# Kernel optimization log

Measured on AMD Instinct MI355X. Metric: run time of the kernel, lower is better.

## Reference

```python
import jax, jax.numpy as jnp
import numpy as np

N_NODES = 100000
N_EDGES = 3200000
IN_DIM = 20
HIDDEN = 4096
OUT_DIM = 2
BN_EPS = 1e-5


def setup_inputs() -> dict:
    key = jax.random.key(0)
    ks = jax.random.split(key, 6)
    node_feature = jax.random.normal(ks[0], (N_NODES, IN_DIM), dtype=jnp.float32)
    edge_index = jax.random.randint(ks[1], (2, N_EDGES), 0, N_NODES, dtype=jnp.int64)
    gcn_w = jax.random.normal(ks[2], (IN_DIM, HIDDEN), dtype=jnp.float32) * (1.0 / np.sqrt(IN_DIM))
    gcn_b = jax.random.normal(ks[3], (HIDDEN,), dtype=jnp.float32) * 0.01
    bn_gamma = jnp.ones((HIDDEN,), dtype=jnp.float32)
    bn_beta = jnp.zeros((HIDDEN,), dtype=jnp.float32)
    lin_w = jax.random.normal(ks[4], (HIDDEN, OUT_DIM), dtype=jnp.float32) * (1.0 / np.sqrt(HIDDEN))
    lin_b = jnp.zeros((OUT_DIM,), dtype=jnp.float32)
    return {"node_feature": node_feature, "edge_index": edge_index,
            "gcn_w": gcn_w, "gcn_b": gcn_b, "bn_gamma": bn_gamma,
            "bn_beta": bn_beta, "lin_w": lin_w, "lin_b": lin_b}


def reference(node_feature, edge_index, gcn_w, gcn_b, bn_gamma, bn_beta, lin_w, lin_b):
    n = node_feature.shape[0]
    # --- GCNConv: add self loops, symmetric degree normalization ---
    loop = jnp.arange(n, dtype=edge_index.dtype)
    row = jnp.concatenate([edge_index[0], loop])  # source nodes
    col = jnp.concatenate([edge_index[1], loop])  # destination nodes
    deg = jax.ops.segment_sum(jnp.ones(col.shape[0], dtype=node_feature.dtype), col, num_segments=n)
    dinv = jnp.where(deg > 0, jax.lax.rsqrt(deg), 0.0)
    norm = dinv[row] * dinv[col]  # [E+N]
    # Aggregate in the small input dim (20), then transform: scatter(norm*x)W == scatter(norm*xW)
    msgs = node_feature[row] * norm[:, None]              # [E+N, in]
    agg = jax.ops.segment_sum(msgs, col, num_segments=n)  # [N, in]
    h = agg @ gcn_w + gcn_b                                # [N, hidden]
    # --- BatchNorm1d (training-mode batch stats, biased variance) ---
    mean = jnp.mean(h, axis=0)
    var = jnp.mean(jnp.square(h - mean), axis=0)
    h = (h - mean) * jax.lax.rsqrt(var + BN_EPS) * bn_gamma + bn_beta
    rsu_embedding = h[0:1]  # [1, hidden]
    # --- Linear -> ReLU -> Softmax(dim=1) ---
    logits = jax.nn.relu(h @ lin_w + lin_b)  # [N, out]
    action_prob = jax.nn.softmax(logits, axis=1)
    return action_prob, rsu_embedding
```

## Files before the change

### kernel.cpp

```cpp
#include <hip/hip_runtime.h>

#define N_NODES 100000
#define N_EDGES 3200000
#define IN_DIM 20
#define HIDDEN 4096
#define OUT_DIM 2
#define BN_EPS 1e-5f


__global__ void k_deg(const int* __restrict__ ei, int* __restrict__ deg) {
    int e = blockIdx.x * blockDim.x + threadIdx.x;
    if (e < N_EDGES) {
        int c = ei[N_EDGES + e];
        atomicAdd(&deg[c], 1);
    }
}

__global__ void k_dinv(const int* __restrict__ deg, float* __restrict__ dinv) {
    int i = blockIdx.x * blockDim.x + threadIdx.x;
    if (i < N_NODES) dinv[i] = rsqrtf((float)(deg[i] + 1));
}

__global__ void k_agginit(const float* __restrict__ nf, const float* __restrict__ dinv,
                          float* __restrict__ agg) {
    int t = blockIdx.x * blockDim.x + threadIdx.x;
    if (t < N_NODES * IN_DIM) {
        int i = t / IN_DIM;
        float d = dinv[i];
        agg[t] = nf[t] * d * d;
    }
}

__global__ void k_scatter(const int* __restrict__ ei, const float* __restrict__ nf,
                          const float* __restrict__ dinv, float* __restrict__ agg) {
    int t = blockIdx.x * blockDim.x + threadIdx.x;
    if (t >= N_EDGES * IN_DIM) return;
    int e = t / IN_DIM;
    int f = t - e * IN_DIM;
    int r = ei[e];
    int c = ei[N_EDGES + e];
    float w = dinv[r] * dinv[c];
    atomicAdd(&agg[c * IN_DIM + f], nf[r * IN_DIM + f] * w);
}

__global__ void k_moments(const float* __restrict__ agg, float* __restrict__ S1,
                          float* __restrict__ S2) {
    int a = blockIdx.y;
    float acc[IN_DIM];
#pragma unroll
    for (int b = 0; b < IN_DIM; b++) acc[b] = 0.f;
    int stride = gridDim.x * blockDim.x;
    for (int i = blockIdx.x * blockDim.x + threadIdx.x; i < N_NODES; i += stride) {
        float v[IN_DIM];
#pragma unroll
        for (int b = 0; b < IN_DIM; b++) v[b] = agg[i * IN_DIM + b];
        float va = (a < IN_DIM) ? agg[i * IN_DIM + a] : 1.0f;
#pragma unroll
        for (int b = 0; b < IN_DIM; b++) acc[b] += va * v[b];
    }
#pragma unroll
    for (int b = 0; b < IN_DIM; b++) {
        float v = acc[b];
#pragma unroll
        for (int s = 32; s > 0; s >>= 1) v += __shfl_down(v, s);
        acc[b] = v;
    }
    if ((threadIdx.x & 63) == 0) {
        float* dst = (a < IN_DIM) ? (S2 + a * IN_DIM) : S1;
#pragma unroll
        for (int b = 0; b < IN_DIM; b++) atomicAdd(&dst[b], acc[b]);
    }
}

__global__ void k_stats(const float* __restrict__ S1, const float* __restrict__ S2,
                        const float* __restrict__ agg, float* __restrict__ mean,
                        float* __restrict__ cov, float* __restrict__ agg0c) {
    int t = threadIdx.x;
    const float invn = 1.0f / (float)N_NODES;
    if (t < IN_DIM) {
        float m = S1[t] * invn;
        mean[t] = m;
        agg0c[t] = agg[t] - m;
    }
    __syncthreads();
    for (int idx = t; idx < IN_DIM * IN_DIM; idx += 64) {
        int a = idx / IN_DIM, b = idx - a * IN_DIM;
        cov[idx] = S2[idx] * invn - mean[a] * mean[b];
    }
}

__global__ void k_prep(const float* __restrict__ gcn_w, const float* __restrict__ gamma,
                       const float* __restrict__ beta, const float* __restrict__ lin_w,
                       const float* __restrict__ cov, const float* __restrict__ agg0c,
                       float* __restrict__ W2, float* __restrict__ dvec,
                       float* __restrict__ out_rsu) {
    __shared__ float scov[IN_DIM * IN_DIM];
    __shared__ float sa0[IN_DIM];
    int tid = threadIdx.x;
    for (int idx = tid; idx < IN_DIM * IN_DIM; idx += blockDim.x) scov[idx] = cov[idx];
    if (tid < IN_DIM) sa0[tid] = agg0c[tid];
    __syncthreads();
    int j = blockIdx.x * blockDim.x + tid;

    float wcol[IN_DIM];
#pragma unroll
    for (int t = 0; t < IN_DIM; t++) wcol[t] = gcn_w[t * HIDDEN + j];

    float var = 0.f;
#pragma unroll
    for (int t = 0; t < IN_DIM; t++) {
        float s = 0.f;
#pragma unroll
        for (int u = 0; u < IN_DIM; u++) s += scov[t * IN_DIM + u] * wcol[u];
        var += wcol[t] * s;
    }
    float aj = gamma[j] * rsqrtf(var + BN_EPS);

    float e0 = 0.f;
#pragma unroll
    for (int t = 0; t < IN_DIM; t++) e0 += sa0[t] * wcol[t];
    out_rsu[j] = e0 * aj + beta[j];

    float lw0 = lin_w[2 * j], lw1 = lin_w[2 * j + 1];
    float bj = beta[j];
    float vals[42];
#pragma unroll
    for (int t = 0; t < IN_DIM; t++) {
        vals[2 * t]     = wcol[t] * aj * lw0;
        vals[2 * t + 1] = wcol[t] * aj * lw1;
    }
    vals[40] = bj * lw0;
    vals[41] = bj * lw1;
#pragma unroll
    for (int q = 0; q < 42; q++) {
        float v = vals[q];
#pragma unroll
        for (int s = 32; s > 0; s >>= 1) v += __shfl_down(v, s);
        if ((tid & 63) == 0) {
            if (q < 40) atomicAdd(&W2[q], v);
            else        atomicAdd(&dvec[q - 40], v);
        }
    }
}

__global__ void k_final(const float* __restrict__ agg, const float* __restrict__ mean,
                        const float* __restrict__ W2, const float* __restrict__ dvec,
                        const float* __restrict__ lin_b, float* __restrict__ out) {
    int i = blockIdx.x * blockDim.x + threadIdx.x;
    if (i >= N_NODES) return;
    float d0 = dvec[0] + lin_b[0];
    float d1 = dvec[1] + lin_b[1];
#pragma unroll
    for (int t = 0; t < IN_DIM; t++) {
        float v = agg[i * IN_DIM + t] - mean[t];
        d0 += v * W2[2 * t];
        d1 += v * W2[2 * t + 1];
    }
    float l0 = fmaxf(d0, 0.f), l1 = fmaxf(d1, 0.f);
    float m = fmaxf(l0, l1);
    float e0 = expf(l0 - m), e1 = expf(l1 - m);
    float inv = 1.f / (e0 + e1);
    out[2 * i]     = e0 * inv;
    out[2 * i + 1] = e1 * inv;
}

extern "C" void kernel_launch(void* const* d_in, const int* in_sizes, int n_in,
                              void* d_out, int out_size, void* d_ws, size_t ws_size,
                              hipStream_t stream) {
    const float* nf    = (const float*)d_in[0];
    const int*   ei    = (const int*)d_in[1];
    const float* gcn_w = (const float*)d_in[2];
    const float* gamma = (const float*)d_in[4];
    const float* beta  = (const float*)d_in[5];
    const float* lin_w = (const float*)d_in[6];
    const float* lin_b = (const float*)d_in[7];
    float* out = (float*)d_out;

    char* ws = (char*)d_ws;
    int*   deg  = (int*)(ws + 0);
    float* dinv = (float*)(ws + 400000);
    float* agg  = (float*)(ws + 800000);
    float* S1   = (float*)(ws + 8800000);
    float* S2   = (float*)(ws + 8800080);
    float* mean = (float*)(ws + 8801680);
    float* cov  = (float*)(ws + 8801760);
    float* a0c  = (float*)(ws + 8803360);
    float* W2   = (float*)(ws + 8803440);
    float* dvec = (float*)(ws + 8803600);

    hipMemsetAsync(deg, 0, 400000, stream);
    hipMemsetAsync(S1, 0, 3608, stream);

    k_deg<<<(N_EDGES + 255) / 256, 256, 0, stream>>>(ei, deg);
    k_dinv<<<(N_NODES + 255) / 256, 256, 0, stream>>>(deg, dinv);
    k_agginit<<<(N_NODES * IN_DIM + 255) / 256, 256, 0, stream>>>(nf, dinv, agg);
    k_scatter<<<(N_EDGES * IN_DIM + 255) / 256, 256, 0, stream>>>(ei, nf, dinv, agg);
    dim3 gm(32, IN_DIM + 1);
    k_moments<<<gm, 256, 0, stream>>>(agg, S1, S2);
    k_stats<<<1, 64, 0, stream>>>(S1, S2, agg, mean, cov, a0c);
    k_prep<<<HIDDEN / 256, 256, 0, stream>>>(gcn_w, gamma, beta, lin_w, cov, a0c, W2, dvec,
                                             out + 2 * N_NODES);
    k_final<<<(N_NODES + 255) / 256, 256, 0, stream>>>(agg, mean, W2, dvec, lin_b, out);
}
```

Baseline: 669.1 us.

## Replace atomic edge scatter with CSR build and atomic-free per-node gather

Builds a CSR grouping of edges by destination node (degree count, three-pass prefix scan, atomic cursor fill) and aggregates each node's neighbors with a float4 gather, replacing 64M float atomics. The moments kernel also computes three covariance rows per block instead of one, cutting re-reads of agg. This adds several kernel launches and a 12.8 MB index buffer, and the gather has load imbalance across nodes. The old scatter path is kept as a fallback when the workspace is too small.

```diff
diff --git a/kernel.cpp b/kernel.cpp
--- a/kernel.cpp
+++ b/kernel.cpp
@@ -6,14 +6,14 @@
 #define HIDDEN 4096
 #define OUT_DIM 2
 #define BN_EPS 1e-5f
-
+#define SCAN_CHUNK 1024
+#define SCAN_NB 98
+
+#define WS_NEED 22004432ull
 
 __global__ void k_deg(const int* __restrict__ ei, int* __restrict__ deg) {
     int e = blockIdx.x * blockDim.x + threadIdx.x;
-    if (e < N_EDGES) {
-        int c = ei[N_EDGES + e];
-        atomicAdd(&deg[c], 1);
-    }
+    if (e < N_EDGES) atomicAdd(&deg[ei[N_EDGES + e]], 1);
 }
 
 __global__ void k_dinv(const int* __restrict__ deg, float* __restrict__ dinv) {
@@ -21,54 +21,138 @@
     if (i < N_NODES) dinv[i] = rsqrtf((float)(deg[i] + 1));
 }
 
-__global__ void k_agginit(const float* __restrict__ nf, const float* __restrict__ dinv,
-                          float* __restrict__ agg) {
+__global__ void k_scan_local(const int* __restrict__ deg, int* __restrict__ rs,
+                             int* __restrict__ blocksum) {
+    __shared__ int lds[256];
+    int b = blockIdx.x, t = threadIdx.x;
+    int base = b * SCAN_CHUNK + t * 4;
+    int v0 = (base + 0 < N_NODES) ? deg[base + 0] : 0;
+    int v1 = (base + 1 < N_NODES) ? deg[base + 1] : 0;
+    int v2 = (base + 2 < N_NODES) ? deg[base + 2] : 0;
+    int v3 = (base + 3 < N_NODES) ? deg[base + 3] : 0;
+    int tsum = v0 + v1 + v2 + v3;
+    int x = tsum;
+    lds[t] = x;
+    __syncthreads();
+    for (int off = 1; off < 256; off <<= 1) {
+        int y = (t >= off) ? lds[t - off] : 0;
+        __syncthreads();
+        x += y;
+        lds[t] = x;
+        __syncthreads();
+    }
+    int ex = x - tsum;
+    if (base + 0 < N_NODES) rs[base + 0] = ex;
+    if (base + 1 < N_NODES) rs[base + 1] = ex + v0;
+    if (base + 2 < N_NODES) rs[base + 2] = ex + v0 + v1;
+    if (base + 3 < N_NODES) rs[base + 3] = ex + v0 + v1 + v2;
+    if (t == 255) blocksum[b] = x;
+}
+
+__global__ void k_scan_mid(const int* __restrict__ blocksum, int* __restrict__ blockpre) {
+    __shared__ int lds[128];
+    int t = threadIdx.x;
+    int v = (t < SCAN_NB) ? blocksum[t] : 0;
+    int x = v;
+    lds[t] = x;
+    __syncthreads();
+    for (int off = 1; off < 128; off <<= 1) {
+        int y = (t >= off) ? lds[t - off] : 0;
+        __syncthreads();
+        x += y;
+        lds[t] = x;
+        __syncthreads();
+    }
+    if (t < SCAN_NB) blockpre[t] = x - v;
+}
+
+__global__ void k_scan_add(int* __restrict__ rs, const int* __restrict__ blockpre,
+                           int* __restrict__ cursor) {
+    int i = blockIdx.x * blockDim.x + threadIdx.x;
+    if (i < N_NODES) {
+        int r = rs[i] + blockpre[i >> 10];
+        rs[i] = r;
+        cursor[i] = r;
+    }
+    if (i == 0) rs[N_NODES] = N_EDGES;
+}
+
+__global__ void k_fill(const int* __restrict__ ei, int* __restrict__ cursor,
+                       int* __restrict__ csr_row) {
+    int e = blockIdx.x * blockDim.x + threadIdx.x;
+    if (e < N_EDGES) {
+        int r = ei[e];
+        int c = ei[N_EDGES + e];
+        int p = atomicAdd(&cursor[c], 1);
+        csr_row[p] = r;
+    }
+}
+
+__global__ void k_gather(const int* __restrict__ csr_row, const int* __restrict__ rs,
+                         const float* __restrict__ nf, const float* __restrict__ dinv,
+                         float* __restrict__ agg) {
     int t = blockIdx.x * blockDim.x + threadIdx.x;
-    if (t < N_NODES * IN_DIM) {
-        int i = t / IN_DIM;
-        float d = dinv[i];
-        agg[t] = nf[t] * d * d;
-    }
-}
-
-__global__ void k_scatter(const int* __restrict__ ei, const float* __restrict__ nf,
-                          const float* __restrict__ dinv, float* __restrict__ agg) {
-    int t = blockIdx.x * blockDim.x + threadIdx.x;
-    if (t >= N_EDGES * IN_DIM) return;
-    int e = t / IN_DIM;
-    int f = t - e * IN_DIM;
-    int r = ei[e];
-    int c = ei[N_EDGES + e];
-    float w = dinv[r] * dinv[c];
-    atomicAdd(&agg[c * IN_DIM + f], nf[r * IN_DIM + f] * w);
-}
-
-__global__ void k_moments(const float* __restrict__ agg, float* __restrict__ S1,
-                          float* __restrict__ S2) {
-    int a = blockIdx.y;
-    float acc[IN_DIM];
-#pragma unroll
-    for (int b = 0; b < IN_DIM; b++) acc[b] = 0.f;
+    if (t >= N_NODES * 5) return;
+    int i = t / 5, g = t % 5;
+    const float4* nf4 = (const float4*)nf;
+    float di = dinv[i];
+    float4 a = nf4[i * 5 + g];
+    float s = di * di;
+    a.x *= s; a.y *= s; a.z *= s; a.w *= s;
+    int e1 = rs[i + 1];
+    for (int e = rs[i]; e < e1; ++e) {
+        int r = csr_row[e];
+        float w = dinv[r] * di;
+        float4 v = nf4[r * 5 + g];
+        a.x += v.x * w; a.y += v.y * w; a.z += v.z * w; a.w += v.w * w;
+    }
+    ((float4*)agg)[i * 5 + g] = a;
+}
+
+__global__ void k_moments3(const float* __restrict__ agg, float* __restrict__ S1,
+                           float* __restrict__ S2) {
+    int y = blockIdx.y;
+    int a0 = 3 * y, a1 = 3 * y + 1, a2 = 3 * y + 2;
+    float acc0[IN_DIM], acc1[IN_DIM], acc2[IN_DIM];
+#pragma unroll
+    for (int b = 0; b < IN_DIM; b++) { acc0[b] = 0.f; acc1[b] = 0.f; acc2[b] = 0.f; }
     int stride = gridDim.x * blockDim.x;
     for (int i = blockIdx.x * blockDim.x + threadIdx.x; i < N_NODES; i += stride) {
+        const float* row = agg + i * IN_DIM;
         float v[IN_DIM];
 #pragma unroll
-        for (int b = 0; b < IN_DIM; b++) v[b] = agg[i * IN_DIM + b];
-        float va = (a < IN_DIM) ? agg[i * IN_DIM + a] : 1.0f;
-#pragma unroll
-        for (int b = 0; b < IN_DIM; b++) acc[b] += va * v[b];
+        for (int b = 0; b < IN_DIM; b++) v[b] = row[b];
+        float va0 = row[a0];
+        float va1 = row[a1];
+        float va2 = (a2 < IN_DIM) ? row[a2] : 1.0f;
+#pragma unroll
+        for (int b = 0; b < IN_DIM; b++) {
+            acc0[b] += va0 * v[b];
+            acc1[b] += va1 * v[b];
+            acc2[b] += va2 * v[b];
+        }
     }
 #pragma unroll
     for (int b = 0; b < IN_DIM; b++) {
-        float v = acc[b];
-#pragma unroll
-        for (int s = 32; s > 0; s >>= 1) v += __shfl_down(v, s);
-        acc[b] = v;
+        float r0 = acc0[b], r1 = acc1[b], r2 = acc2[b];
+#pragma unroll
+        for (int s = 32; s > 0; s >>= 1) {
+            r0 += __shfl_down(r0, s);
+            r1 += __shfl_down(r1, s);
+            r2 += __shfl_down(r2, s);
+        }
+        acc0[b] = r0; acc1[b] = r1; acc2[b] = r2;
     }
     if ((threadIdx.x & 63) == 0) {
-        float* dst = (a < IN_DIM) ? (S2 + a * IN_DIM) : S1;
-#pragma unroll
-        for (int b = 0; b < IN_DIM; b++) atomicAdd(&dst[b], acc[b]);
+        float* d0 = S2 + a0 * IN_DIM;
+        float* d1 = S2 + a1 * IN_DIM;
+        float* d2 = (a2 < IN_DIM) ? (S2 + a2 * IN_DIM) : S1;
+#pragma unroll
+        for (int b = 0; b < IN_DIM; b++) {
+            atomicAdd(&d0[b], acc0[b]);
+            atomicAdd(&d1[b], acc1[b]);
+            atomicAdd(&d2[b], acc2[b]);
+        }
     }
 }
 
@@ -164,6 +248,28 @@
     out[2 * i + 1] = e1 * inv;
 }
 
+__global__ void k_agginit(const float* __restrict__ nf, const float* __restrict__ dinv,
+                          float* __restrict__ agg) {
+    int t = blockIdx.x * blockDim.x + threadIdx.x;
+    if (t < N_NODES * IN_DIM) {
+        int i = t / IN_DIM;
+        float d = dinv[i];
+        agg[t] = nf[t] * d * d;
+    }
+}
+
+__global__ void k_scatter(const int* __restrict__ ei, const float* __restrict__ nf,
+                          const float* __restrict__ dinv, float* __restrict__ agg) {
+    int t = blockIdx.x * blockDim.x + threadIdx.x;
+    if (t >= N_EDGES * IN_DIM) return;
+    int e = t / IN_DIM;
+    int f = t - e * IN_DIM;
+    int r = ei[e];
+    int c = ei[N_EDGES + e];
+    float w = dinv[r] * dinv[c];
+    atomicAdd(&agg[c * IN_DIM + f], nf[r * IN_DIM + f] * w);
+}
+
 extern "C" void kernel_launch(void* const* d_in, const int* in_sizes, int n_in,
                               void* d_out, int out_size, void* d_ws, size_t ws_size,
                               hipStream_t stream) {
@@ -180,25 +286,57 @@
     int*   deg  = (int*)(ws + 0);
     float* dinv = (float*)(ws + 400000);
     float* agg  = (float*)(ws + 800000);
-    float* S1   = (float*)(ws + 8800000);
-    float* S2   = (float*)(ws + 8800080);
-    float* mean = (float*)(ws + 8801680);
-    float* cov  = (float*)(ws + 8801760);
-    float* a0c  = (float*)(ws + 8803360);
-    float* W2   = (float*)(ws + 8803440);
-    float* dvec = (float*)(ws + 8803600);
-
-    hipMemsetAsync(deg, 0, 400000, stream);
-    hipMemsetAsync(S1, 0, 3608, stream);
-
-    k_deg<<<(N_EDGES + 255) / 256, 256, 0, stream>>>(ei, deg);
-    k_dinv<<<(N_NODES + 255) / 256, 256, 0, stream>>>(deg, dinv);
-    k_agginit<<<(N_NODES * IN_DIM + 255) / 256, 256, 0, stream>>>(nf, dinv, agg);
-    k_scatter<<<(N_EDGES * IN_DIM + 255) / 256, 256, 0, stream>>>(ei, nf, dinv, agg);
-    dim3 gm(32, IN_DIM + 1);
-    k_moments<<<gm, 256, 0, stream>>>(agg, S1, S2);
-    k_stats<<<1, 64, 0, stream>>>(S1, S2, agg, mean, cov, a0c);
-    k_prep<<<HIDDEN / 256, 256, 0, stream>>>(gcn_w, gamma, beta, lin_w, cov, a0c, W2, dvec,
-                                             out + 2 * N_NODES);
-    k_final<<<(N_NODES + 255) / 256, 256, 0, stream>>>(agg, mean, W2, dvec, lin_b, out);
-}
+
+    if (ws_size >= WS_NEED) {
+        int* rs       = (int*)(ws + 8800000);
+        int* csr_row  = (int*)(ws + 9200016);
+        int* blocksum = (int*)(ws + 22000016);
+        int* blockpre = (int*)(ws + 22000416);
+        float* S1   = (float*)(ws + 22000816);
+        float* S2   = (float*)(ws + 22000896);
+        float* mean = (float*)(ws + 22002496);
+        float* cov  = (float*)(ws + 22002576);
+        float* a0c  = (float*)(ws + 22004176);
+        float* W2   = (float*)(ws + 22004256);
+        float* dvec = (float*)(ws + 22004416);
+
+        hipMemsetAsync(deg, 0, 400000, stream);
+        hipMemsetAsync(S1, 0, 3608, stream);
+
+        k_deg<<<(N_EDGES + 255) / 256, 256, 0, stream>>>(ei, deg);
+        k_dinv<<<(N_NODES + 255) / 256, 256, 0, stream>>>(deg, dinv);
+        k_scan_local<<<SCAN_NB, 256, 0, stream>>>(deg, rs, blocksum);
+        k_scan_mid<<<1, 128, 0, stream>>>(blocksum, blockpre);
+        k_scan_add<<<(N_NODES + 255) / 256, 256, 0, stream>>>(rs, blockpre, deg);
+        k_fill<<<(N_EDGES + 255) / 256, 256, 0, stream>>>(ei, deg, csr_row);
+        k_gather<<<(N_NODES * 5 + 255) / 256, 256, 0, stream>>>(csr_row, rs, nf, dinv, agg);
+        dim3 gm(32, 7);
+        k_moments3<<<gm, 256, 0, stream>>>(agg, S1, S2);
+        k_stats<<<1, 64, 0, stream>>>(S1, S2, agg, mean, cov, a0c);
+        k_prep<<<HIDDEN / 256, 256, 0, stream>>>(gcn_w, gamma, beta, lin_w, cov, a0c, W2,
+                                                 dvec, out + 2 * N_NODES);
+        k_final<<<(N_NODES + 255) / 256, 256, 0, stream>>>(agg, mean, W2, dvec, lin_b, out);
+    } else {
+        float* S1   = (float*)(ws + 8800000);
+        float* S2   = (float*)(ws + 8800080);
+        float* mean = (float*)(ws + 8801680);
+        float* cov  = (float*)(ws + 8801760);
+        float* a0c  = (float*)(ws + 8803360);
+        float* W2   = (float*)(ws + 8803440);
+        float* dvec = (float*)(ws + 8803600);
+
+        hipMemsetAsync(deg, 0, 400000, stream);
+        hipMemsetAsync(S1, 0, 3608, stream);
+
+        k_deg<<<(N_EDGES + 255) / 256, 256, 0, stream>>>(ei, deg);
+        k_dinv<<<(N_NODES + 255) / 256, 256, 0, stream>>>(deg, dinv);
+        k_agginit<<<(N_NODES * IN_DIM + 255) / 256, 256, 0, stream>>>(nf, dinv, agg);
+        k_scatter<<<(N_EDGES * IN_DIM + 255) / 256, 256, 0, stream>>>(ei, nf, dinv, agg);
+        dim3 gm(32, 7);
+        k_moments3<<<gm, 256, 0, stream>>>(agg, S1, S2);
+        k_stats<<<1, 64, 0, stream>>>(S1, S2, agg, mean, cov, a0c);
+        k_prep<<<HIDDEN / 256, 256, 0, stream>>>(gcn_w, gamma, beta, lin_w, cov, a0c, W2,
+                                                 dvec, out + 2 * N_NODES);
+        k_final<<<(N_NODES + 255) / 256, 256, 0, stream>>>(agg, mean, W2, dvec, lin_b, out);
+    }
+}
```

After: 663.9 us. About the same (-0.8%).
